# Kernel tuning notes

Measured on AMD Instinct MI355X. Metric: run time of the kernel, lower is better.

The kernel has to match this reference:

```python
import jax, jax.numpy as jnp
import numpy as np
from jax import lax

# LNS semantics: values are held as (sign, log_base|x|); exact conversion round-trips
# make log-domain mul/add mathematically identical to float conv/linear/relu, so the
# faithful reference is the equivalent float pipeline.

def _conv(x, w, b):
    # x: [B,C,H,W], w: [O,C,kh,kw] (torch layout), stride 1, no padding
    y = lax.conv_general_dilated(x, w, window_strides=(1, 1), padding='VALID',
                                 dimension_numbers=('NCHW', 'OIHW', 'NCHW'))
    return y + b[None, :, None, None]

def _maxpool2(x):
    return lax.reduce_window(x, -jnp.inf, lax.max,
                             window_dimensions=(1, 1, 2, 2),
                             window_strides=(1, 1, 2, 2), padding='VALID')

def setup_inputs() -> dict:
    key = jax.random.key(0)
    ks = jax.random.split(key, 9)
    s = lambda k, shape, fan: jax.random.normal(k, shape, jnp.float32) * (1.0 / np.sqrt(fan))
    return {
        'x': jax.random.normal(ks[0], (512, 1, 54, 54), jnp.float32),
        'conv1_w': s(ks[1], (32, 1, 3, 3), 9),
        'conv1_b': s(ks[2], (32,), 9),
        'conv2_w': s(ks[3], (64, 32, 3, 3), 32 * 9),
        'conv2_b': s(ks[4], (64,), 32 * 9),
        'fc1_w': s(ks[5], (128, 9216), 9216),
        'fc1_b': s(ks[6], (128,), 9216),
        'fc2_w': s(ks[7], (10, 128), 128),
        'fc2_b': s(ks[8], (10,), 128),
    }

def reference(x, conv1_w, conv1_b, conv2_w, conv2_b, fc1_w, fc1_b, fc2_w, fc2_b):
    h = jnp.maximum(_conv(x, conv1_w, conv1_b), 0.0)          # [B,32,52,52]
    h = _maxpool2(h)                                          # [B,32,26,26]
    h = jnp.maximum(_conv(h, conv2_w, conv2_b), 0.0)          # [B,64,24,24]
    h = _maxpool2(h)                                          # [B,64,12,12]
    h = h.reshape(h.shape[0], -1)                             # [B,9216]
    h = jnp.maximum(h @ fc1_w.T + fc1_b, 0.0)                 # [B,128]
    return h @ fc2_w.T + fc2_b                                # [B,10]
```

## Files before the change

### kernel.cpp

```cpp
#include <hip/hip_runtime.h>


#define B 512
#define POS 676
#define ICP 36
#define P2SZ (64*12*12)

typedef unsigned short ushort_t;
typedef ushort_t ushort4v __attribute__((ext_vector_type(4)));
typedef short s16x8 __attribute__((ext_vector_type(8)));
typedef float f32x4 __attribute__((ext_vector_type(4)));
typedef float f32x2 __attribute__((ext_vector_type(2)));

__device__ __forceinline__ ushort_t f2bf(float f) {
    union { float f; unsigned u; } a; a.f = f;
    unsigned r = a.u + 0x7FFFu + ((a.u >> 16) & 1u);
    return (ushort_t)(r >> 16);
}
__device__ __forceinline__ float bf2f(ushort_t u) {
    union { unsigned u; float f; } a; a.u = ((unsigned)u) << 16;
    return a.f;
}

#define N_WR (64 * 9 * 32)
#define N_WF (128 * 9216)
#define CONV1_BLOCKS 3328
#define PREP_BLOCKS  4680

__global__ __launch_bounds__(256) void conv1_prep(const float* __restrict__ x,
                                                  const float* __restrict__ w,
                                                  const float* __restrict__ bias,
                                                  const float* __restrict__ c2w,
                                                  const float* __restrict__ f1w,
                                                  ushort_t* __restrict__ out,
                                                  ushort_t* __restrict__ wr,
                                                  ushort_t* __restrict__ wfb) {
    int blk = blockIdx.x;
    if (blk >= CONV1_BLOCKS) {
        int t = (blk - CONV1_BLOCKS) * 256 + threadIdx.x;
        if (t < N_WR) {
            int ic  = t & 31;
            int tap = (t >> 5) % 9;
            int oc  = t / 288;
            wr[t] = f2bf(c2w[oc * 288 + ic * 9 + tap]);
        } else if (t < N_WR + N_WF) {
            int i  = t - N_WR;
            int oc  = i & 63;
            int pos = (i >> 6) % 144;
            int n   = i / 9216;
            wfb[i] = f2bf(f1w[(size_t)n * 9216 + oc * 144 + pos]);
        }
        return;
    }
    int t = blk * 256 + threadIdx.x;
    int ic = t & 31;
    int r  = t >> 5;
    int h  = r & 1;
    int r2 = r >> 1;
    int py = r2 % 26;
    int b  = r2 / 26;
    int px0 = h * 13;

    const float* wp = w + ic * 9;
    float w00 = wp[0], w01 = wp[1], w02 = wp[2];
    float w10 = wp[3], w11 = wp[4], w12 = wp[5];
    float w20 = wp[6], w21 = wp[7], w22 = wp[8];
    float bv = bias[ic];

    const float* xr = x + b * (54 * 54) + (2 * py) * 54 + 2 * px0;
    ushort_t* po = out + ((size_t)b * POS + py * 26 + px0) * 32 + ic;

    f32x2 p[4], q[4];
#pragma unroll
    for (int rr = 0; rr < 4; ++rr) p[rr] = *reinterpret_cast<const f32x2*>(xr + rr * 54);
#pragma unroll
    for (int rr = 0; rr < 4; ++rr) q[rr] = *reinterpret_cast<const f32x2*>(xr + rr * 54 + 2);

#pragma unroll
    for (int j = 0; j < 13; ++j) {
        f32x2 mid[4];
#pragma unroll
        for (int rr = 0; rr < 4; ++rr) mid[rr] = (f32x2){p[rr].y, q[rr].x};

        f32x2 s0 = p[0] * (f32x2)w00 + mid[0] * (f32x2)w01 + q[0] * (f32x2)w02
                 + p[1] * (f32x2)w10 + mid[1] * (f32x2)w11 + q[1] * (f32x2)w12
                 + p[2] * (f32x2)w20 + mid[2] * (f32x2)w21 + q[2] * (f32x2)w22;
        f32x2 s1 = p[1] * (f32x2)w00 + mid[1] * (f32x2)w01 + q[1] * (f32x2)w02
                 + p[2] * (f32x2)w10 + mid[2] * (f32x2)w11 + q[2] * (f32x2)w12
                 + p[3] * (f32x2)w20 + mid[3] * (f32x2)w21 + q[3] * (f32x2)w22;

        float m = fmaxf(fmaxf(s0.x, s0.y), fmaxf(s1.x, s1.y));
        po[j * 32] = f2bf(fmaxf(m + bv, 0.0f));
        if (j < 12) {
#pragma unroll
            for (int rr = 0; rr < 4; ++rr) {
                p[rr] = q[rr];
                q[rr] = *reinterpret_cast<const f32x2*>(xr + rr * 54 + 2 * j + 4);
            }
        }
    }
}

__global__ __launch_bounds__(256) void conv2_mfma(const ushort_t* __restrict__ p1,
                                                  const ushort_t* __restrict__ wr,
                                                  const float* __restrict__ bias,
                                                  ushort_t* __restrict__ pool2cl) {
    __shared__ ushort_t lds[260 * ICP];
    int blk = blockIdx.x;
    int b = blk / 3, c = blk % 3;
    int tid = threadIdx.x;

    const ushort_t* src = p1 + ((size_t)b * POS + 8 * c * 26) * 32;
    for (int t = tid; t < 260 * 8; t += 256) {
        int pos = t >> 3, off = (t & 7) * 4;
        ushort4v v = *reinterpret_cast<const ushort4v*>(src + pos * 32 + off);
        *reinterpret_cast<ushort4v*>(&lds[pos * ICP + off]) = v;
    }
    __syncthreads();

    int lane = tid & 63, wid = tid >> 6;
    int quad = lane >> 4, lr = lane & 15;

    int ebase[3];
#pragma unroll
    for (int t = 0; t < 3; ++t) {
        int m  = t * 16 + lr;
        int yl = m / 24;
        int xx = m - yl * 24;
        ebase[t] = ((2 * wid + yl) * 26 + xx) * ICP + quad * 8;
    }

    f32x4 acc[3][4];
#pragma unroll
    for (int t = 0; t < 3; ++t)
#pragma unroll
        for (int n = 0; n < 4; ++n) acc[t][n] = (f32x4){0.f, 0.f, 0.f, 0.f};

    const ushort_t* wb = wr + (size_t)lr * 288 + quad * 8;

#pragma unroll
    for (int tap = 0; tap < 9; ++tap) {
        int ky = tap / 3, kx = tap % 3;
        int koff = (ky * 26 + kx) * ICP;
        s16x8 a[3];
#pragma unroll
        for (int t = 0; t < 3; ++t) {
            union { ushort4v s[2]; s16x8 v; } u;
            u.s[0] = *reinterpret_cast<const ushort4v*>(&lds[ebase[t] + koff]);
            u.s[1] = *reinterpret_cast<const ushort4v*>(&lds[ebase[t] + koff + 4]);
            a[t] = u.v;
        }
        s16x8 bf[4];
#pragma unroll
        for (int n = 0; n < 4; ++n)
            bf[n] = *reinterpret_cast<const s16x8*>(wb + n * 4608 + tap * 32);
#pragma unroll
        for (int t = 0; t < 3; ++t)
#pragma unroll
            for (int n = 0; n < 4; ++n)
                acc[t][n] = __builtin_amdgcn_mfma_f32_16x16x32_bf16(a[t], bf[n], acc[t][n], 0, 0, 0);
    }
    __syncthreads();

    ushort_t* scr = lds + wid * 1536;
#pragma unroll
    for (int t = 0; t < 3; ++t)
#pragma unroll
        for (int n = 0; n < 4; ++n) {
            int oc = n * 16 + lr;
            int i0 = t * 8 + quad * 2;
            float v0 = fmaxf(acc[t][n][0], acc[t][n][1]);
            float v1 = fmaxf(acc[t][n][2], acc[t][n][3]);
            union { ushort_t u2[2]; unsigned w; } pk;
            pk.u2[0] = f2bf(v0); pk.u2[1] = f2bf(v1);
            *reinterpret_cast<unsigned*>(&scr[oc * 24 + i0]) = pk.w;
        }
    int oc = lane;
    const ushort_t* row = scr + oc * 24;
    float bv = bias[oc];
    int py = c * 4 + wid;
    ushort_t* po = pool2cl + ((size_t)b * 144 + py * 12) * 64 + oc;
#pragma unroll
    for (int px = 0; px < 12; ++px) {
        float r0 = bf2f(row[px]);
        float r1 = bf2f(row[px + 12]);
        po[px * 64] = f2bf(fmaxf(fmaxf(r0, r1) + bv, 0.0f));
    }
}

__global__ __launch_bounds__(256) void fc1_mfma(const ushort_t* __restrict__ A,
                                                 const ushort_t* __restrict__ W,
                                                 float* __restrict__ Cpart) {
    int tid = threadIdx.x;
    int lane = tid & 63, wid = tid >> 6;
    int lr = lane & 15, quad = lane >> 4;
    int w  = blockIdx.x * 4 + wid;
    int nt = w & 3;
    int ks = (w >> 2) & 31;
    int mt = w >> 7;

    int m0 = mt * 32;
    int n0 = nt * 32;
    int k0 = ks * 288 + quad * 8;
    const ushort_t* a0 = A + (size_t)(m0 + lr) * 9216 + k0;
    const ushort_t* a1 = a0 + (size_t)16 * 9216;
    const ushort_t* b0 = W + (size_t)(n0 + lr) * 9216 + k0;
    const ushort_t* b1 = b0 + (size_t)16 * 9216;

    f32x4 acc[2][2];
#pragma unroll
    for (int i = 0; i < 2; ++i)
#pragma unroll
        for (int j = 0; j < 2; ++j) acc[i][j] = (f32x4){0.f, 0.f, 0.f, 0.f};

#pragma unroll
    for (int kk = 0; kk < 9; ++kk) {
        s16x8 av0 = *reinterpret_cast<const s16x8*>(a0 + kk * 32);
        s16x8 av1 = *reinterpret_cast<const s16x8*>(a1 + kk * 32);
        s16x8 bv0 = *reinterpret_cast<const s16x8*>(b0 + kk * 32);
        s16x8 bv1 = *reinterpret_cast<const s16x8*>(b1 + kk * 32);
        acc[0][0] = __builtin_amdgcn_mfma_f32_16x16x32_bf16(av0, bv0, acc[0][0], 0, 0, 0);
        acc[0][1] = __builtin_amdgcn_mfma_f32_16x16x32_bf16(av0, bv1, acc[0][1], 0, 0, 0);
        acc[1][0] = __builtin_amdgcn_mfma_f32_16x16x32_bf16(av1, bv0, acc[1][0], 0, 0, 0);
        acc[1][1] = __builtin_amdgcn_mfma_f32_16x16x32_bf16(av1, bv1, acc[1][1], 0, 0, 0);
    }

    float* cp = Cpart + (size_t)ks * (512 * 128);
#pragma unroll
    for (int i = 0; i < 2; ++i) {
        int crow = m0 + i * 16 + quad * 4;
#pragma unroll
        for (int j = 0; j < 2; ++j) {
            int col = n0 + j * 16 + lr;
#pragma unroll
            for (int r = 0; r < 4; ++r)
                cp[(size_t)(crow + r) * 128 + col] = acc[i][j][r];
        }
    }
}

__global__ __launch_bounds__(128) void fc1fc2(const float* __restrict__ Cpart,
                                              const float* __restrict__ b1,
                                              const float* __restrict__ w2,
                                              const float* __restrict__ b2,
                                              float* __restrict__ out) {
    __shared__ float h[128];
    int b = blockIdx.x, k = threadIdx.x;
    float s = 0.f;
#pragma unroll
    for (int ks = 0; ks < 32; ++ks) s += Cpart[(size_t)ks * (512 * 128) + b * 128 + k];
    h[k] = fmaxf(s + b1[k], 0.0f);
    __syncthreads();
    if (k < 10) {
        const float* wp = w2 + k * 128;
        float acc = 0.f;
#pragma unroll 8
        for (int j = 0; j < 128; ++j) acc += h[j] * wp[j];
        out[b * 10 + k] = acc + b2[k];
    }
}

extern "C" void kernel_launch(void* const* d_in, const int* in_sizes, int n_in,
                              void* d_out, int out_size, void* d_ws, size_t ws_size,
                              hipStream_t stream) {
    const float* x       = (const float*)d_in[0];
    const float* conv1_w = (const float*)d_in[1];
    const float* conv1_b = (const float*)d_in[2];
    const float* conv2_w = (const float*)d_in[3];
    const float* conv2_b = (const float*)d_in[4];
    const float* fc1_w   = (const float*)d_in[5];
    const float* fc1_b   = (const float*)d_in[6];
    const float* fc2_w   = (const float*)d_in[7];
    const float* fc2_b   = (const float*)d_in[8];
    float* out = (float*)d_out;

    char* ws = (char*)d_ws;
    ushort_t* pool1 = (ushort_t*)ws;
    ws += (size_t)B * POS * 32 * sizeof(ushort_t);
    ushort_t* wr = (ushort_t*)ws;
    ws += N_WR * sizeof(ushort_t) + 128;
    ushort_t* wfb = (ushort_t*)ws;
    ws += N_WF * sizeof(ushort_t) + 128;
    ushort_t* pool2cl = (ushort_t*)ws;
    ws += (size_t)B * P2SZ * sizeof(ushort_t) + 128;
    float* Cpart = (float*)ws;
    ws += (size_t)32 * 512 * 128 * sizeof(float) + 128;

    {
        conv1_prep<<<CONV1_BLOCKS + PREP_BLOCKS, 256, 0, stream>>>(
            x, conv1_w, conv1_b, conv2_w, fc1_w, pool1, wr, wfb);
    }
    {
        conv2_mfma<<<B * 3, 256, 0, stream>>>(pool1, wr, conv2_b, pool2cl);
    }
    {
        fc1_mfma<<<512, 256, 0, stream>>>(pool2cl, wfb, Cpart);
    }
    {
        fc1fc2<<<B, 128, 0, stream>>>(Cpart, fc1_b, fc2_w, fc2_b, out);
    }
}
```

Before: 131.2 us.

## Fuse fc1 split-K reduction and fc2 via last-block atomic counter; pad conv2 scratch

Merges the fc1 split-K GEMM and the fc1-reduce/relu/fc2 kernel into one launch. Each block now owns one 32-row M tile and one K slice across all four N tiles, and the last block to finish a given M tile (found with an atomic counter) sums the 32 partials and computes fc2. The counters are zeroed in the prep kernel. This removes one kernel launch and its dependency gap, but the final reduction now runs on only 16 blocks instead of 512. Separately, the conv2 LDS scratch row stride goes from 24 to 26 to reduce bank conflicts.

```diff
diff --git a/kernel.cpp b/kernel.cpp
--- a/kernel.cpp
+++ b/kernel.cpp
@@ -5,6 +5,7 @@
 #define POS 676
 #define ICP 36
 #define P2SZ (64*12*12)
+#define SCR 26
 
 typedef unsigned short ushort_t;
 typedef ushort_t ushort4v __attribute__((ext_vector_type(4)));
@@ -34,9 +35,11 @@
                                                   const float* __restrict__ f1w,
                                                   ushort_t* __restrict__ out,
                                                   ushort_t* __restrict__ wr,
-                                                  ushort_t* __restrict__ wfb) {
+                                                  ushort_t* __restrict__ wfb,
+                                                  unsigned* __restrict__ done) {
     int blk = blockIdx.x;
     if (blk >= CONV1_BLOCKS) {
+        if (blk == CONV1_BLOCKS && threadIdx.x < 16) done[threadIdx.x] = 0u;
         int t = (blk - CONV1_BLOCKS) * 256 + threadIdx.x;
         if (t < N_WR) {
             int ic  = t & 31;
@@ -162,7 +165,7 @@
     }
     __syncthreads();
 
-    ushort_t* scr = lds + wid * 1536;
+    ushort_t* scr = lds + wid * (64 * SCR);
 #pragma unroll
     for (int t = 0; t < 3; ++t)
 #pragma unroll
@@ -173,10 +176,10 @@
             float v1 = fmaxf(acc[t][n][2], acc[t][n][3]);
             union { ushort_t u2[2]; unsigned w; } pk;
             pk.u2[0] = f2bf(v0); pk.u2[1] = f2bf(v1);
-            *reinterpret_cast<unsigned*>(&scr[oc * 24 + i0]) = pk.w;
+            *reinterpret_cast<unsigned*>(&scr[oc * SCR + i0]) = pk.w;
         }
     int oc = lane;
-    const ushort_t* row = scr + oc * 24;
+    const ushort_t* row = scr + oc * SCR;
     float bv = bias[oc];
     int py = c * 4 + wid;
     ushort_t* po = pool2cl + ((size_t)b * 144 + py * 12) * 64 + oc;
@@ -188,24 +191,28 @@
     }
 }
 
-__global__ __launch_bounds__(256) void fc1_mfma(const ushort_t* __restrict__ A,
-                                                 const ushort_t* __restrict__ W,
-                                                 float* __restrict__ Cpart) {
+__global__ __launch_bounds__(256) void fc1fc2_fused(const ushort_t* __restrict__ A,
+                                                    const ushort_t* __restrict__ W,
+                                                    const float* __restrict__ b1,
+                                                    const float* __restrict__ w2,
+                                                    const float* __restrict__ b2,
+                                                    float* __restrict__ Cpart,
+                                                    float* __restrict__ out,
+                                                    unsigned* __restrict__ done) {
+    int blk = blockIdx.x;
+    int mt = blk >> 5;
+    int ks = blk & 31;
     int tid = threadIdx.x;
     int lane = tid & 63, wid = tid >> 6;
     int lr = lane & 15, quad = lane >> 4;
-    int w  = blockIdx.x * 4 + wid;
-    int nt = w & 3;
-    int ks = (w >> 2) & 31;
-    int mt = w >> 7;
 
     int m0 = mt * 32;
-    int n0 = nt * 32;
+    int n0 = wid * 32;
     int k0 = ks * 288 + quad * 8;
     const ushort_t* a0 = A + (size_t)(m0 + lr) * 9216 + k0;
     const ushort_t* a1 = a0 + (size_t)16 * 9216;
-    const ushort_t* b0 = W + (size_t)(n0 + lr) * 9216 + k0;
-    const ushort_t* b1 = b0 + (size_t)16 * 9216;
+    const ushort_t* bp0 = W + (size_t)(n0 + lr) * 9216 + k0;
+    const ushort_t* bp1 = bp0 + (size_t)16 * 9216;
 
     f32x4 acc[2][2];
 #pragma unroll
@@ -217,8 +224,8 @@
     for (int kk = 0; kk < 9; ++kk) {
         s16x8 av0 = *reinterpret_cast<const s16x8*>(a0 + kk * 32);
         s16x8 av1 = *reinterpret_cast<const s16x8*>(a1 + kk * 32);
-        s16x8 bv0 = *reinterpret_cast<const s16x8*>(b0 + kk * 32);
-        s16x8 bv1 = *reinterpret_cast<const s16x8*>(b1 + kk * 32);
+        s16x8 bv0 = *reinterpret_cast<const s16x8*>(bp0 + kk * 32);
+        s16x8 bv1 = *reinterpret_cast<const s16x8*>(bp1 + kk * 32);
         acc[0][0] = __builtin_amdgcn_mfma_f32_16x16x32_bf16(av0, bv0, acc[0][0], 0, 0, 0);
         acc[0][1] = __builtin_amdgcn_mfma_f32_16x16x32_bf16(av0, bv1, acc[0][1], 0, 0, 0);
         acc[1][0] = __builtin_amdgcn_mfma_f32_16x16x32_bf16(av1, bv0, acc[1][0], 0, 0, 0);
@@ -237,26 +244,33 @@
                 cp[(size_t)(crow + r) * 128 + col] = acc[i][j][r];
         }
     }
-}
-
-__global__ __launch_bounds__(128) void fc1fc2(const float* __restrict__ Cpart,
-                                              const float* __restrict__ b1,
-                                              const float* __restrict__ w2,
-                                              const float* __restrict__ b2,
-                                              float* __restrict__ out) {
-    __shared__ float h[128];
-    int b = blockIdx.x, k = threadIdx.x;
-    float s = 0.f;
-#pragma unroll
-    for (int ks = 0; ks < 32; ++ks) s += Cpart[(size_t)ks * (512 * 128) + b * 128 + k];
-    h[k] = fmaxf(s + b1[k], 0.0f);
-    __syncthreads();
-    if (k < 10) {
-        const float* wp = w2 + k * 128;
-        float acc = 0.f;
+
+    __threadfence();
+    __syncthreads();
+    __shared__ unsigned is_last;
+    if (tid == 0)
+        is_last = (atomicAdd(&done[mt], 1u) == 31u) ? 1u : 0u;
+    __syncthreads();
+    if (!is_last) return;
+    __threadfence();
+
+    __shared__ float h[32][128];
+    for (int idx = tid; idx < 32 * 128; idx += 256) {
+        int mm = idx >> 7, nn = idx & 127;
+        float s = 0.f;
+#pragma unroll
+        for (int k2 = 0; k2 < 32; ++k2)
+            s += Cpart[(size_t)k2 * (512 * 128) + (size_t)(m0 + mm) * 128 + nn];
+        h[mm][nn] = fmaxf(s + b1[nn], 0.0f);
+    }
+    __syncthreads();
+    for (int idx = tid; idx < 32 * 10; idx += 256) {
+        int mm = idx / 10, o = idx % 10;
+        const float* wp = w2 + o * 128;
+        float a2 = 0.f;
 #pragma unroll 8
-        for (int j = 0; j < 128; ++j) acc += h[j] * wp[j];
-        out[b * 10 + k] = acc + b2[k];
+        for (int j = 0; j < 128; ++j) a2 += h[mm][j] * wp[j];
+        out[(m0 + mm) * 10 + o] = a2 + b2[o];
     }
 }
 
@@ -285,18 +299,12 @@
     ws += (size_t)B * P2SZ * sizeof(ushort_t) + 128;
     float* Cpart = (float*)ws;
     ws += (size_t)32 * 512 * 128 * sizeof(float) + 128;
-
-    {
-        conv1_prep<<<CONV1_BLOCKS + PREP_BLOCKS, 256, 0, stream>>>(
-            x, conv1_w, conv1_b, conv2_w, fc1_w, pool1, wr, wfb);
-    }
-    {
-        conv2_mfma<<<B * 3, 256, 0, stream>>>(pool1, wr, conv2_b, pool2cl);
-    }
-    {
-        fc1_mfma<<<512, 256, 0, stream>>>(pool2cl, wfb, Cpart);
-    }
-    {
-        fc1fc2<<<B, 128, 0, stream>>>(Cpart, fc1_b, fc2_w, fc2_b, out);
-    }
-}
+    unsigned* done = (unsigned*)ws;
+    ws += 256;
+
+    conv1_prep<<<CONV1_BLOCKS + PREP_BLOCKS, 256, 0, stream>>>(
+        x, conv1_w, conv1_b, conv2_w, fc1_w, pool1, wr, wfb, done);
+    conv2_mfma<<<B * 3, 256, 0, stream>>>(pool1, wr, conv2_b, pool2cl);
+    fc1fc2_fused<<<512, 256, 0, stream>>>(pool2cl, wfb, fc1_b, fc2_w, fc2_b,
+                                          Cpart, out, done);
+}
```

After: 267.7 us. 2.04x slower.
